# Kernel tuning notes

Measured on AMD Instinct MI355X. Metric: run time of the kernel, lower is better.

The kernel has to match this reference:

```python
import jax, jax.numpy as jnp
import numpy as np

N_HEAD = 16
RMS_EPS = 1.1920928955078125e-07  # torch F.rms_norm default eps = finfo(fp32).eps


def _rope_tables(seq_len, head_dim, dtype):
    steps = jnp.arange(seq_len, dtype=jnp.float32)
    rates = 10000.0 ** (-jnp.arange(0, head_dim, 2, dtype=jnp.float32) / head_dim)
    angles = jnp.outer(steps, rates)  # [S, D/2]
    return jnp.cos(angles).astype(dtype)[None, None], jnp.sin(angles).astype(dtype)[None, None]


def _apply_rotary(x, cos, sin):
    # interleaved RoPE: pairs (x[2i], x[2i+1]) rotated
    left = x[..., ::2]
    right = x[..., 1::2]
    lo = left * cos - right * sin
    ro = left * sin + right * cos
    return jnp.stack((lo, ro), axis=-1).reshape(x.shape)


def _rms_norm(x, eps=RMS_EPS):
    ms = jnp.mean(jnp.square(x), axis=-1, keepdims=True)
    return x * jax.lax.rsqrt(ms + eps)


def setup_inputs() -> dict:
    key = jax.random.key(0)
    k1, k2, k3 = jax.random.split(key, 3)
    B, S, E = 2, 2048, 2048
    x = jax.random.normal(k1, (B, S, E), dtype=jnp.float32)
    w_qkv = jax.random.normal(k2, (3 * E, E), dtype=jnp.float32) * (E ** -0.5)
    w_proj = jax.random.normal(k3, (E, E), dtype=jnp.float32) * (E ** -0.5)
    return {"x": x, "w_qkv": w_qkv, "w_proj": w_proj}


def reference(x, w_qkv, w_proj):
    B, S, E = x.shape
    H = N_HEAD
    D = E // H

    qkv = x @ w_qkv.T  # [B, S, 3E]
    q, k, v = jnp.split(qkv, 3, axis=-1)
    # [B, S, E] -> [B, H, S, D]
    q = q.reshape(B, S, H, D).transpose(0, 2, 1, 3)
    k = k.reshape(B, S, H, D).transpose(0, 2, 1, 3)
    v = v.reshape(B, S, H, D).transpose(0, 2, 1, 3)

    cos, sin = _rope_tables(S, D, x.dtype)  # [1,1,S,D/2]
    q = _apply_rotary(q, cos, sin)
    k = _apply_rotary(k, cos, sin)

    q = _rms_norm(q)
    k = _rms_norm(k)

    scale = 1.0 / jnp.sqrt(jnp.asarray(D, dtype=x.dtype))
    scores = jnp.einsum("bhqd,bhkd->bhqk", q, k) * scale  # [B,H,S,S]
    causal = jnp.tril(jnp.ones((S, S), dtype=bool))
    scores = jnp.where(causal[None, None], scores, jnp.asarray(-jnp.inf, dtype=scores.dtype))
    attn = jax.nn.softmax(scores, axis=-1)
    y = jnp.einsum("bhqk,bhkd->bhqd", attn, v)  # [B,H,S,D]
    y = y.transpose(0, 2, 1, 3).reshape(B, S, E)
    return y @ w_proj.T
```

## Files before the change

### kernel.cpp

```cpp
#include <hip/hip_runtime.h>

typedef unsigned short ushort_t;
using bf16x8 = __attribute__((ext_vector_type(8))) short;
using u16x8  = __attribute__((ext_vector_type(8))) unsigned short;
using f32x4  = __attribute__((ext_vector_type(4))) float;

#define DEV static __device__ __forceinline__

DEV unsigned short f2bf(float f) {
  union { float f; unsigned u; } a; a.f = f;
  unsigned r = a.u + 0x7fffu + ((a.u >> 16) & 1u);
  return (unsigned short)(r >> 16);
}
DEV float bf2f(unsigned short u) {
  union { unsigned u; float f; } a; a.u = ((unsigned)u) << 16;
  return a.f;
}
DEV void load_lds16(const void* g, void* l) {
  __builtin_amdgcn_global_load_lds(
      (const __attribute__((address_space(1))) void*)g,
      (__attribute__((address_space(3))) void*)l, 16, 0, 0);
}

__global__ __launch_bounds__(256) void cast_kernel(
    const float* __restrict__ src, ushort_t* __restrict__ dst, int n4) {
  int i = blockIdx.x * 256 + threadIdx.x;
  if (i >= n4) return;
  float4 f = ((const float4*)src)[i];
  ushort4 o;
  o.x = f2bf(f.x); o.y = f2bf(f.y); o.z = f2bf(f.z); o.w = f2bf(f.w);
  ((ushort4*)dst)[i] = o;
}

__global__ __launch_bounds__(256) void rope_tables_kernel(float* __restrict__ tab) {
  int idx = blockIdx.x * 256 + threadIdx.x;
  int s = idx >> 6, i = idx & 63;
  float rate = exp2f(-13.287712379549449f * ((float)(2 * i) * (1.0f / 128.0f)));
  float ang = (float)s * rate;
  tab[idx * 2]     = cosf(ang);
  tab[idx * 2 + 1] = sinf(ang);
}

template<int OUTF32>
__global__ __launch_bounds__(256) void gemm_bt(
    const ushort_t* __restrict__ A, const ushort_t* __restrict__ B,
    void* __restrict__ C, int M, int N, int K) {
  __shared__ __align__(16) ushort_t sA[128 * 32];
  __shared__ __align__(16) ushort_t sB[128 * 32];
  const int tid  = threadIdx.x;
  const int wave = tid >> 6;
  const int lane = tid & 63;
  const int lrow = lane & 15;
  const int lk   = lane >> 4;
  const int bm = blockIdx.y * 128;
  const int bn = blockIdx.x * 128;
  const int wrow = (wave >> 1) * 64;
  const int wcol = (wave & 1) * 64;

  f32x4 acc[4][4];
#pragma unroll
  for (int r = 0; r < 4; ++r)
#pragma unroll
    for (int c = 0; c < 4; ++c) acc[r][c] = (f32x4){0.f, 0.f, 0.f, 0.f};

  const int sRow0 = wave * 32 + (lane >> 2);
  const int sRow1 = sRow0 + 16;
  const int sSwz  = ((lane & 3) * 16) ^ ((sRow0 & 3) << 4);
  const char* aS0 = (const char*)A + (size_t)(bm + sRow0) * (size_t)(K * 2) + sSwz;
  const char* aS1 = (const char*)A + (size_t)(bm + sRow1) * (size_t)(K * 2) + sSwz;
  const char* bS0 = (const char*)B + (size_t)(bn + sRow0) * (size_t)(K * 2) + sSwz;
  const char* bS1 = (const char*)B + (size_t)(bn + sRow1) * (size_t)(K * 2) + sSwz;
  char* aD0 = (char*)sA + wave * 2048 + lane * 16;
  char* aD1 = aD0 + 1024;
  char* bD0 = (char*)sB + wave * 2048 + lane * 16;
  char* bD1 = bD0 + 1024;

  int offA[4], offB[4];
  const int fSwz = (lk * 16) ^ ((lrow & 3) << 4);
#pragma unroll
  for (int r = 0; r < 4; ++r) offA[r] = (wrow + r * 16 + lrow) * 64 + fSwz;
#pragma unroll
  for (int c = 0; c < 4; ++c) offB[c] = (wcol + c * 16 + lrow) * 64 + fSwz;

  const int nk = K >> 5;
  for (int ks = 0; ks < nk; ++ks) {
    const size_t koff = (size_t)ks * 64;
    load_lds16(aS0 + koff, aD0);
    load_lds16(aS1 + koff, aD1);
    load_lds16(bS0 + koff, bD0);
    load_lds16(bS1 + koff, bD1);
    __syncthreads();
    bf16x8 af[4], bv[4];
#pragma unroll
    for (int r = 0; r < 4; ++r) af[r] = *(const bf16x8*)((const char*)sA + offA[r]);
#pragma unroll
    for (int c = 0; c < 4; ++c) bv[c] = *(const bf16x8*)((const char*)sB + offB[c]);
#pragma unroll
    for (int r = 0; r < 4; ++r)
#pragma unroll
      for (int c = 0; c < 4; ++c)
        acc[r][c] = __builtin_amdgcn_mfma_f32_16x16x32_bf16(af[r], bv[c], acc[r][c], 0, 0, 0);
    __syncthreads();
  }

#pragma unroll
  for (int r = 0; r < 4; ++r)
#pragma unroll
    for (int i = 0; i < 4; ++i) {
      const size_t row = (size_t)(bm + wrow + r * 16 + lk * 4 + i);
#pragma unroll
      for (int c = 0; c < 4; ++c) {
        const size_t col = (size_t)(bn + wcol + c * 16 + lrow);
        float v = acc[r][c][i];
        if (OUTF32) ((float*)C)[row * (size_t)N + col] = v;
        else        ((ushort_t*)C)[row * (size_t)N + col] = f2bf(v);
      }
    }
}

__global__ __launch_bounds__(256) void rope_rms_kernel(
    const ushort_t* __restrict__ qkv, ushort_t* __restrict__ q,
    ushort_t* __restrict__ k, ushort_t* __restrict__ vt,
    const float* __restrict__ tab) {
  const int lane = threadIdx.x & 63;
  const int row  = blockIdx.x * 4 + (threadIdx.x >> 6);
  const int h = row & 15;
  int t = row >> 4;
  const int which = t % 3; t /= 3;
  const int s = t & 2047;
  const int b = t >> 11;
  const size_t src = ((size_t)(b * 2048 + s)) * 6144 + which * 2048 + h * 128 + lane * 2;
  ushort2 xv = *(const ushort2*)&qkv[src];
  if (which == 2) {
    size_t vbase = ((size_t)((b * 16 + h) * 128 + lane * 2)) * 2048 + s;
    vt[vbase]        = xv.x;
    vt[vbase + 2048] = xv.y;
    return;
  }
  float lo = bf2f(xv.x), ro = bf2f(xv.y);
  const float2 cs = *(const float2*)&tab[(s * 64 + lane) * 2];
  float l2 = lo * cs.x - ro * cs.y;
  float r2 = lo * cs.y + ro * cs.x;
  float ss = l2 * l2 + r2 * r2;
#pragma unroll
  for (int off = 1; off < 64; off <<= 1) ss += __shfl_xor(ss, off);
  float inv = rsqrtf(ss * (1.0f / 128.0f) + 1.1920928955078125e-07f);
  if (which == 0) inv *= 0.1275174398f;
  lo = l2 * inv; ro = r2 * inv;
  ushort_t* dst = (which == 0) ? q : k;
  ushort2 o; o.x = f2bf(lo); o.y = f2bf(ro);
  *(ushort2*)&dst[(((size_t)(b * 16 + h)) * 2048 + s) * 128 + lane * 2] = o;
}

__global__ __launch_bounds__(256) void attn_kernel(
    const ushort_t* __restrict__ Q, const ushort_t* __restrict__ K,
    const ushort_t* __restrict__ VT, ushort_t* __restrict__ Y) {
  __shared__ __align__(16) ushort_t sK[64 * 128];
  __shared__ __align__(16) ushort_t sV[128 * 64];
  const int bh = blockIdx.x;
  const int yp = blockIdx.y;
  const int wave = threadIdx.x >> 6, lane = threadIdx.x & 63;
  const int ql = lane & 15, lk = lane >> 4;
  const size_t hq = (size_t)bh * 2048 * 128;
  const int b = bh >> 4, h = bh & 15;

  const char* kB = (const char*)(K + hq);
  const char* vB = (const char*)(VT + hq);
  const char* kSrc[4]; char* kDst[4];
  const char* vSrc[4]; char* vDst[4];
#pragma unroll
  for (int t = 0; t < 4; ++t) {
    int r = wave * 16 + t * 4 + (lane >> 4);
    int kgr = r >> 4, lkr = (r >> 2) & 3, ir = r & 3;
    int rho = (kgr >> 1) * 32 + lkr * 8 + (kgr & 1) * 4 + ir;
    kSrc[t] = kB + rho * 256 + (((lane & 15) * 16) ^ ((r & 7) << 4));
    kDst[t] = (char*)sK + (wave * 256 + t * 64 + lane) * 16;
    int d = wave * 32 + t * 8 + (lane >> 3);
    vSrc[t] = vB + (size_t)d * 4096 + (((lane & 7) * 16) ^ ((d & 7) << 4));
    vDst[t] = (char*)sV + (wave * 256 + t * 64 + lane) * 16;
  }

  for (int pass = 0; pass < 2; ++pass) {
    const int qt = pass ? (31 - yp) : yp;
    const int q = qt * 64 + wave * 16 + ql;

    bf16x8 qf[4];
#pragma unroll
    for (int ks = 0; ks < 4; ++ks)
      qf[ks] = *(const bf16x8*)&Q[hq + (size_t)q * 128 + ks * 32 + lk * 8];

    f32x4 acc[8];
#pragma unroll
    for (int g = 0; g < 8; ++g) acc[g] = (f32x4){0.f, 0.f, 0.f, 0.f};
    float mrow = -3.0e38f, lsum = 0.f;

    for (int kt = 0; kt <= qt; ++kt) {
#pragma unroll
      for (int t = 0; t < 4; ++t) {
        load_lds16(kSrc[t] + (size_t)kt * 16384, kDst[t]);
        load_lds16(vSrc[t] + kt * 128, vDst[t]);
      }
      __syncthreads();

      f32x4 st[4];
#pragma unroll
      for (int kg = 0; kg < 4; ++kg) st[kg] = (f32x4){0.f, 0.f, 0.f, 0.f};
#pragma unroll
      for (int kg = 0; kg < 4; ++kg) {
        const int row = kg * 16 + ql;
        const int rswz = (row & 7) << 4;
#pragma unroll
        for (int ks = 0; ks < 4; ++ks) {
          bf16x8 kf = *(const bf16x8*)((const char*)sK + row * 256 + ((ks * 64 + lk * 16) ^ rswz));
          st[kg] = __builtin_amdgcn_mfma_f32_16x16x32_bf16(kf, qf[ks], st[kg], 0, 0, 0);
        }
      }
      float sv[4][4]; float mp = -3.0e38f;
#pragma unroll
      for (int kg = 0; kg < 4; ++kg) {
        const int kl = ((kg >> 1) << 5) + lk * 8 + ((kg & 1) << 2);
#pragma unroll
        for (int i = 0; i < 4; ++i) {
          const int key = kt * 64 + kl + i;
          float v = (key <= q) ? st[kg][i] : -3.0e38f;
          sv[kg][i] = v;
          mp = fmaxf(mp, v);
        }
      }
      mp = fmaxf(mp, __shfl_xor(mp, 16));
      mp = fmaxf(mp, __shfl_xor(mp, 32));
      const float mn = fmaxf(mrow, mp);
      const float corr = exp2f(mrow - mn);
      mrow = mn;
      float p[4][4]; float rs = 0.f;
#pragma unroll
      for (int kg = 0; kg < 4; ++kg)
#pragma unroll
        for (int i = 0; i < 4; ++i) {
          float e = exp2f(sv[kg][i] - mn);
          p[kg][i] = e; rs += e;
        }
      rs += __shfl_xor(rs, 16);
      rs += __shfl_xor(rs, 32);
      lsum = lsum * corr + rs;
#pragma unroll
      for (int g = 0; g < 8; ++g)
#pragma unroll
        for (int i = 0; i < 4; ++i) acc[g][i] *= corr;
      bf16x8 pb[2];
#pragma unroll
      for (int c = 0; c < 2; ++c) {
        union { bf16x8 v; ushort_t u[8]; } pk;
#pragma unroll
        for (int j = 0; j < 8; ++j) pk.u[j] = f2bf(p[2 * c + (j >> 2)][j & 3]);
        pb[c] = pk.v;
      }
#pragma unroll
      for (int dg = 0; dg < 8; ++dg) {
        const int d = dg * 16 + ql;
        const int dswz = (d & 7) << 4;
#pragma unroll
        for (int c = 0; c < 2; ++c) {
          bf16x8 vf = *(const bf16x8*)((const char*)sV + d * 128 + ((c * 64 + lk * 16) ^ dswz));
          acc[dg] = __builtin_amdgcn_mfma_f32_16x16x32_bf16(vf, pb[c], acc[dg], 0, 0, 0);
        }
      }
      __syncthreads();
    }

    const float inv = 1.0f / lsum;
    const size_t orow = ((size_t)(b * 2048 + q)) * 2048 + h * 128;
#pragma unroll
    for (int dg = 0; dg < 8; ++dg) {
      ushort4 o;
      o.x = f2bf(acc[dg][0] * inv);
      o.y = f2bf(acc[dg][1] * inv);
      o.z = f2bf(acc[dg][2] * inv);
      o.w = f2bf(acc[dg][3] * inv);
      *(ushort4*)&Y[orow + dg * 16 + lk * 4] = o;
    }
  }
}

extern "C" void kernel_launch(void* const* d_in, const int* in_sizes, int n_in,
                              void* d_out, int out_size, void* d_ws, size_t ws_size,
                              hipStream_t stream) {
  const float* x     = (const float*)d_in[0];
  const float* wqkv  = (const float*)d_in[1];
  const float* wproj = (const float*)d_in[2];
  float* out = (float*)d_out;
  char* ws = (char*)d_ws;

  ushort_t* x_bf     = (ushort_t*)(ws);
  ushort_t* wqkv_bf  = (ushort_t*)(ws + 16777216);
  ushort_t* wproj_bf = (ushort_t*)(ws + 41943040);
  ushort_t* qkv_bf   = (ushort_t*)(ws + 50331648);
  ushort_t* q_bf     = (ushort_t*)(ws + 100663296);
  ushort_t* k_bf     = (ushort_t*)(ws + 117440512);
  ushort_t* vt_bf    = (ushort_t*)(ws + 134217728);
  float*    tab      = (float*)(ws + 150994944);
  if (ws_size < 152043520u) return;

  cast_kernel<<<8192, 256, 0, stream>>>(x, x_bf, 2097152);
  cast_kernel<<<12288, 256, 0, stream>>>(wqkv, wqkv_bf, 3145728);
  cast_kernel<<<4096, 256, 0, stream>>>(wproj, wproj_bf, 1048576);
  rope_tables_kernel<<<512, 256, 0, stream>>>(tab);

  gemm_bt<0><<<dim3(48, 32), 256, 0, stream>>>(x_bf, wqkv_bf, qkv_bf, 4096, 6144, 2048);

  rope_rms_kernel<<<49152, 256, 0, stream>>>(qkv_bf, q_bf, k_bf, vt_bf, tab);

  attn_kernel<<<dim3(32, 16), 256, 0, stream>>>(q_bf, k_bf, vt_bf, qkv_bf );

  gemm_bt<1><<<dim3(16, 32), 256, 0, stream>>>(qkv_bf, wproj_bf, out, 4096, 2048, 2048);
}
```

Baseline: 344.7 us.

## Double-buffer GEMM and attention loads, enlarge tiles, remap GEMM workgroups

Replaces the GEMM with a templated kernel that double-buffers LDS tiles, so the next K-slice is fetched while MFMAs run. It uses a 256x128 tile for the QKV projection, remaps workgroup IDs for cache locality, and raises wave priority around the MFMA block. The attention kernel also double-buffers K/V tiles and has each wave process two 16-query groups (128 queries per block), reusing each K/V fragment across both. This cuts LDS traffic and sync stalls per FLOP, at the cost of more registers and LDS and lower occupancy.

```diff
diff --git a/kernel.cpp b/kernel.cpp
--- a/kernel.cpp
+++ b/kernel.cpp
@@ -2,7 +2,6 @@
 
 typedef unsigned short ushort_t;
 using bf16x8 = __attribute__((ext_vector_type(8))) short;
-using u16x8  = __attribute__((ext_vector_type(8))) unsigned short;
 using f32x4  = __attribute__((ext_vector_type(4))) float;
 
 #define DEV static __device__ __forceinline__
@@ -41,77 +40,106 @@
   tab[idx * 2 + 1] = sinf(ang);
 }
 
-template<int OUTF32>
-__global__ __launch_bounds__(256) void gemm_bt(
-    const ushort_t* __restrict__ A, const ushort_t* __restrict__ B,
+template<int BM, int BN, int OUTF32>
+__global__ __launch_bounds__(256, 2) void gemm_bal(
+    const ushort_t* __restrict__ A, const ushort_t* __restrict__ Bm,
     void* __restrict__ C, int M, int N, int K) {
-  __shared__ __align__(16) ushort_t sA[128 * 32];
-  __shared__ __align__(16) ushort_t sB[128 * 32];
-  const int tid  = threadIdx.x;
+  constexpr int MF   = BM / 32;
+  constexpr int NF   = BN / 32;
+  constexpr int NCA  = BM / 64;
+  constexpr int NCB  = BN / 64;
+  constexpr int NC   = NCA + NCB;
+  constexpr int ABY  = BM * 64;
+  constexpr int BUFB = (BM + BN) * 64;
+  __shared__ __align__(16) char lds[2 * BUFB];
+
+  const int nby = M / BM;
+  const int nwg = nby * (N / BN);
+  const int orig = blockIdx.x;
+  const int wgid = (orig & 7) * (nwg >> 3) + (orig >> 3);
+  const int bm = (wgid % nby) * BM;
+  const int bn = (wgid / nby) * BN;
+
+  const int tid = threadIdx.x;
+  const int lane = tid & 63;
   const int wave = tid >> 6;
-  const int lane = tid & 63;
-  const int lrow = lane & 15;
-  const int lk   = lane >> 4;
-  const int bm = blockIdx.y * 128;
-  const int bn = blockIdx.x * 128;
-  const int wrow = (wave >> 1) * 64;
-  const int wcol = (wave & 1) * 64;
-
-  f32x4 acc[4][4];
-#pragma unroll
-  for (int r = 0; r < 4; ++r)
-#pragma unroll
-    for (int c = 0; c < 4; ++c) acc[r][c] = (f32x4){0.f, 0.f, 0.f, 0.f};
-
-  const int sRow0 = wave * 32 + (lane >> 2);
-  const int sRow1 = sRow0 + 16;
-  const int sSwz  = ((lane & 3) * 16) ^ ((sRow0 & 3) << 4);
-  const char* aS0 = (const char*)A + (size_t)(bm + sRow0) * (size_t)(K * 2) + sSwz;
-  const char* aS1 = (const char*)A + (size_t)(bm + sRow1) * (size_t)(K * 2) + sSwz;
-  const char* bS0 = (const char*)B + (size_t)(bn + sRow0) * (size_t)(K * 2) + sSwz;
-  const char* bS1 = (const char*)B + (size_t)(bn + sRow1) * (size_t)(K * 2) + sSwz;
-  char* aD0 = (char*)sA + wave * 2048 + lane * 16;
-  char* aD1 = aD0 + 1024;
-  char* bD0 = (char*)sB + wave * 2048 + lane * 16;
-  char* bD1 = bD0 + 1024;
-
-  int offA[4], offB[4];
-  const int fSwz = (lk * 16) ^ ((lrow & 3) << 4);
-#pragma unroll
-  for (int r = 0; r < 4; ++r) offA[r] = (wrow + r * 16 + lrow) * 64 + fSwz;
-#pragma unroll
-  for (int c = 0; c < 4; ++c) offB[c] = (wcol + c * 16 + lrow) * 64 + fSwz;
-
-  const int nk = K >> 5;
-  for (int ks = 0; ks < nk; ++ks) {
-    const size_t koff = (size_t)ks * 64;
-    load_lds16(aS0 + koff, aD0);
-    load_lds16(aS1 + koff, aD1);
-    load_lds16(bS0 + koff, bD0);
-    load_lds16(bS1 + koff, bD1);
+  const int ql = lane & 15, lk = lane >> 4;
+  const int wm = wave >> 1, wn = wave & 1;
+
+  f32x4 acc[MF][NF];
+#pragma unroll
+  for (int m = 0; m < MF; ++m)
+#pragma unroll
+    for (int n = 0; n < NF; ++n) acc[m][n] = (f32x4){0.f, 0.f, 0.f, 0.f};
+
+  const int rin  = tid >> 2;
+  const int sswz = ((tid & 3) ^ ((rin >> 1) & 3)) * 16;
+  const size_t rb = (size_t)K * 2;
+  const char* src[NC];
+#pragma unroll
+  for (int c = 0; c < NCA; ++c)
+    src[c] = (const char*)A + (size_t)(bm + c * 64 + rin) * rb + sswz;
+#pragma unroll
+  for (int c = 0; c < NCB; ++c)
+    src[NCA + c] = (const char*)Bm + (size_t)(bn + c * 64 + rin) * rb + sswz;
+  char* const ldsc = (char*)lds;
+  const int dT = tid * 16;
+
+  int aOff[MF], bOff[NF];
+#pragma unroll
+  for (int m = 0; m < MF; ++m) {
+    const int r = wm * (BM / 2) + m * 16 + ql;
+    aOff[m] = r * 64 + ((lk ^ ((r >> 1) & 3)) * 16);
+  }
+#pragma unroll
+  for (int n = 0; n < NF; ++n) {
+    const int r = wn * (BN / 2) + n * 16 + ql;
+    bOff[n] = ABY + r * 64 + ((lk ^ ((r >> 1) & 3)) * 16);
+  }
+
+#define STAGE(BB, KT) do {                                   \
+    char* d_ = ldsc + (BB) * BUFB + dT;                      \
+    const size_t ko_ = (size_t)(KT) * 64;                    \
+    _Pragma("unroll")                                        \
+    for (int c = 0; c < NC; ++c)                             \
+      load_lds16(src[c] + ko_, d_ + c * 4096);               \
+  } while (0)
+#define MFMA(a, b, c) __builtin_amdgcn_mfma_f32_16x16x32_bf16(a, b, c, 0, 0, 0)
+
+  const int ns = K >> 5;
+  STAGE(0, 0);
+  __syncthreads();
+
+  for (int t = 0; t < ns; ++t) {
+    const int nk = (t + 1 < ns) ? t + 1 : t;
+    STAGE((t + 1) & 1, nk);
+    const char* sb = ldsc + (t & 1) * BUFB;
+    bf16x8 bF[NF], aF[MF];
+#pragma unroll
+    for (int n = 0; n < NF; ++n) bF[n] = *(const bf16x8*)(sb + bOff[n]);
+#pragma unroll
+    for (int m = 0; m < MF; ++m) aF[m] = *(const bf16x8*)(sb + aOff[m]);
+    __builtin_amdgcn_s_setprio(1);
+#pragma unroll
+    for (int m = 0; m < MF; ++m)
+#pragma unroll
+      for (int n = 0; n < NF; ++n)
+        acc[m][n] = MFMA(aF[m], bF[n], acc[m][n]);
+    __builtin_amdgcn_s_setprio(0);
     __syncthreads();
-    bf16x8 af[4], bv[4];
-#pragma unroll
-    for (int r = 0; r < 4; ++r) af[r] = *(const bf16x8*)((const char*)sA + offA[r]);
-#pragma unroll
-    for (int c = 0; c < 4; ++c) bv[c] = *(const bf16x8*)((const char*)sB + offB[c]);
-#pragma unroll
-    for (int r = 0; r < 4; ++r)
-#pragma unroll
-      for (int c = 0; c < 4; ++c)
-        acc[r][c] = __builtin_amdgcn_mfma_f32_16x16x32_bf16(af[r], bv[c], acc[r][c], 0, 0, 0);
-    __syncthreads();
-  }
-
-#pragma unroll
-  for (int r = 0; r < 4; ++r)
+  }
+#undef STAGE
+#undef MFMA
+
+#pragma unroll
+  for (int m = 0; m < MF; ++m)
 #pragma unroll
     for (int i = 0; i < 4; ++i) {
-      const size_t row = (size_t)(bm + wrow + r * 16 + lk * 4 + i);
-#pragma unroll
-      for (int c = 0; c < 4; ++c) {
-        const size_t col = (size_t)(bn + wcol + c * 16 + lrow);
-        float v = acc[r][c][i];
+      const size_t row = (size_t)(bm + wm * (BM / 2) + m * 16 + lk * 4 + i);
+#pragma unroll
+      for (int n = 0; n < NF; ++n) {
+        const size_t col = (size_t)(bn + wn * (BN / 2) + n * 16 + ql);
+        float v = acc[m][n][i];
         if (OUTF32) ((float*)C)[row * (size_t)N + col] = v;
         else        ((ushort_t*)C)[row * (size_t)N + col] = f2bf(v);
       }
@@ -152,11 +180,11 @@
   *(ushort2*)&dst[(((size_t)(b * 16 + h)) * 2048 + s) * 128 + lane * 2] = o;
 }
 
-__global__ __launch_bounds__(256) void attn_kernel(
+__global__ __launch_bounds__(256, 1) void attn_kernel(
     const ushort_t* __restrict__ Q, const ushort_t* __restrict__ K,
     const ushort_t* __restrict__ VT, ushort_t* __restrict__ Y) {
-  __shared__ __align__(16) ushort_t sK[64 * 128];
-  __shared__ __align__(16) ushort_t sV[128 * 64];
+  __shared__ __align__(16) ushort_t sK[2][64 * 128];
+  __shared__ __align__(16) ushort_t sV[2][128 * 64];
   const int bh = blockIdx.x;
   const int yp = blockIdx.y;
   const int wave = threadIdx.x >> 6, lane = threadIdx.x & 63;
@@ -180,80 +208,102 @@
     vDst[t] = (char*)sV + (wave * 256 + t * 64 + lane) * 16;
   }
 
+#define STAGEKV(KT, BB) do {                                         \
+    _Pragma("unroll")                                                \
+    for (int t_ = 0; t_ < 4; ++t_) {                                 \
+      load_lds16(kSrc[t_] + (size_t)(KT) * 16384, kDst[t_] + (BB) * 16384); \
+      load_lds16(vSrc[t_] + (KT) * 128, vDst[t_] + (BB) * 16384);    \
+    }                                                                \
+  } while (0)
+
+  int buf = 0;
+  STAGEKV(0, 0);
+  __syncthreads();
+
   for (int pass = 0; pass < 2; ++pass) {
-    const int qt = pass ? (31 - yp) : yp;
-    const int q = qt * 64 + wave * 16 + ql;
-
-    bf16x8 qf[4];
-#pragma unroll
-    for (int ks = 0; ks < 4; ++ks)
-      qf[ks] = *(const bf16x8*)&Q[hq + (size_t)q * 128 + ks * 32 + lk * 8];
-
-    f32x4 acc[8];
-#pragma unroll
-    for (int g = 0; g < 8; ++g) acc[g] = (f32x4){0.f, 0.f, 0.f, 0.f};
-    float mrow = -3.0e38f, lsum = 0.f;
-
-    for (int kt = 0; kt <= qt; ++kt) {
-#pragma unroll
-      for (int t = 0; t < 4; ++t) {
-        load_lds16(kSrc[t] + (size_t)kt * 16384, kDst[t]);
-        load_lds16(vSrc[t] + kt * 128, vDst[t]);
-      }
-      __syncthreads();
-
-      f32x4 st[4];
-#pragma unroll
-      for (int kg = 0; kg < 4; ++kg) st[kg] = (f32x4){0.f, 0.f, 0.f, 0.f};
+    const int qt = pass ? (15 - yp) : yp;
+    const int ktmax = 2 * qt + 1;
+    const int q0 = qt * 128 + wave * 32 + ql;
+
+    bf16x8 qf[2][4];
+#pragma unroll
+    for (int g = 0; g < 2; ++g)
+#pragma unroll
+      for (int ks = 0; ks < 4; ++ks)
+        qf[g][ks] = *(const bf16x8*)&Q[hq + (size_t)(q0 + g * 16) * 128 + ks * 32 + lk * 8];
+
+    f32x4 acc[2][8];
+#pragma unroll
+    for (int g = 0; g < 2; ++g)
+#pragma unroll
+      for (int dg = 0; dg < 8; ++dg) acc[g][dg] = (f32x4){0.f, 0.f, 0.f, 0.f};
+    float mrow[2] = {-3.0e38f, -3.0e38f}, lsum[2] = {0.f, 0.f};
+
+    for (int kt = 0; kt <= ktmax; ++kt) {
+      const int nk = (kt < ktmax) ? kt + 1 : (pass == 0 ? 0 : ktmax);
+      STAGEKV(nk, buf ^ 1);
+      const char* sKb = (const char*)sK + buf * 16384;
+      const char* sVb = (const char*)sV + buf * 16384;
+
+      f32x4 st[2][4];
+#pragma unroll
+      for (int g = 0; g < 2; ++g)
+#pragma unroll
+        for (int kg = 0; kg < 4; ++kg) st[g][kg] = (f32x4){0.f, 0.f, 0.f, 0.f};
 #pragma unroll
       for (int kg = 0; kg < 4; ++kg) {
         const int row = kg * 16 + ql;
         const int rswz = (row & 7) << 4;
 #pragma unroll
         for (int ks = 0; ks < 4; ++ks) {
-          bf16x8 kf = *(const bf16x8*)((const char*)sK + row * 256 + ((ks * 64 + lk * 16) ^ rswz));
-          st[kg] = __builtin_amdgcn_mfma_f32_16x16x32_bf16(kf, qf[ks], st[kg], 0, 0, 0);
+          bf16x8 kf = *(const bf16x8*)(sKb + row * 256 + ((ks * 64 + lk * 16) ^ rswz));
+          st[0][kg] = __builtin_amdgcn_mfma_f32_16x16x32_bf16(kf, qf[0][ks], st[0][kg], 0, 0, 0);
+          st[1][kg] = __builtin_amdgcn_mfma_f32_16x16x32_bf16(kf, qf[1][ks], st[1][kg], 0, 0, 0);
         }
       }
-      float sv[4][4]; float mp = -3.0e38f;
-#pragma unroll
-      for (int kg = 0; kg < 4; ++kg) {
-        const int kl = ((kg >> 1) << 5) + lk * 8 + ((kg & 1) << 2);
-#pragma unroll
-        for (int i = 0; i < 4; ++i) {
-          const int key = kt * 64 + kl + i;
-          float v = (key <= q) ? st[kg][i] : -3.0e38f;
-          sv[kg][i] = v;
-          mp = fmaxf(mp, v);
+      bf16x8 pb[2][2];
+#pragma unroll
+      for (int g = 0; g < 2; ++g) {
+        const int q = q0 + g * 16;
+        float sv[4][4]; float mp = -3.0e38f;
+#pragma unroll
+        for (int kg = 0; kg < 4; ++kg) {
+          const int kl = ((kg >> 1) << 5) + lk * 8 + ((kg & 1) << 2);
+#pragma unroll
+          for (int i = 0; i < 4; ++i) {
+            const int key = kt * 64 + kl + i;
+            float v = (key <= q) ? st[g][kg][i] : -3.0e38f;
+            sv[kg][i] = v;
+            mp = fmaxf(mp, v);
+          }
         }
-      }
-      mp = fmaxf(mp, __shfl_xor(mp, 16));
-      mp = fmaxf(mp, __shfl_xor(mp, 32));
-      const float mn = fmaxf(mrow, mp);
-      const float corr = exp2f(mrow - mn);
-      mrow = mn;
-      float p[4][4]; float rs = 0.f;
-#pragma unroll
-      for (int kg = 0; kg < 4; ++kg)
-#pragma unroll
-        for (int i = 0; i < 4; ++i) {
-          float e = exp2f(sv[kg][i] - mn);
-          p[kg][i] = e; rs += e;
+        mp = fmaxf(mp, __shfl_xor(mp, 16));
+        mp = fmaxf(mp, __shfl_xor(mp, 32));
+        const float mn = fmaxf(mrow[g], mp);
+        const float corr = exp2f(mrow[g] - mn);
+        mrow[g] = mn;
+        float p[4][4]; float rs = 0.f;
+#pragma unroll
+        for (int kg = 0; kg < 4; ++kg)
+#pragma unroll
+          for (int i = 0; i < 4; ++i) {
+            float e = exp2f(sv[kg][i] - mn);
+            p[kg][i] = e; rs += e;
+          }
+        rs += __shfl_xor(rs, 16);
+        rs += __shfl_xor(rs, 32);
+        lsum[g] = lsum[g] * corr + rs;
+#pragma unroll
+        for (int dg = 0; dg < 8; ++dg)
+#pragma unroll
+          for (int i = 0; i < 4; ++i) acc[g][dg][i] *= corr;
+#pragma unroll
+        for (int c = 0; c < 2; ++c) {
+          union { bf16x8 v; ushort_t u[8]; } pk;
+#pragma unroll
+          for (int j = 0; j < 8; ++j) pk.u[j] = f2bf(p[2 * c + (j >> 2)][j & 3]);
+          pb[g][c] = pk.v;
         }
-      rs += __shfl_xor(rs, 16);
-      rs += __shfl_xor(rs, 32);
-      lsum = lsum * corr + rs;
-#pragma unroll
-      for (int g = 0; g < 8; ++g)
-#pragma unroll
-        for (int i = 0; i < 4; ++i) acc[g][i] *= corr;
-      bf16x8 pb[2];
-#pragma unroll
-      for (int c = 0; c < 2; ++c) {
-        union { bf16x8 v; ushort_t u[8]; } pk;
-#pragma unroll
-        for (int j = 0; j < 8; ++j) pk.u[j] = f2bf(p[2 * c + (j >> 2)][j & 3]);
-        pb[c] = pk.v;
       }
 #pragma unroll
       for (int dg = 0; dg < 8; ++dg) {
@@ -261,25 +311,31 @@
         const int dswz = (d & 7) << 4;
 #pragma unroll
         for (int c = 0; c < 2; ++c) {
-          bf16x8 vf = *(const bf16x8*)((const char*)sV + d * 128 + ((c * 64 + lk * 16) ^ dswz));
-          acc[dg] = __builtin_amdgcn_mfma_f32_16x16x32_bf16(vf, pb[c], acc[dg], 0, 0, 0);
+          bf16x8 vf = *(const bf16x8*)(sVb + d * 128 + ((c * 64 + lk * 16) ^ dswz));
+          acc[0][dg] = __builtin_amdgcn_mfma_f32_16x16x32_bf16(vf, pb[0][c], acc[0][dg], 0, 0, 0);
+          acc[1][dg] = __builtin_amdgcn_mfma_f32_16x16x32_bf16(vf, pb[1][c], acc[1][dg], 0, 0, 0);
         }
       }
       __syncthreads();
+      buf ^= 1;
     }
 
-    const float inv = 1.0f / lsum;
-    const size_t orow = ((size_t)(b * 2048 + q)) * 2048 + h * 128;
-#pragma unroll
-    for (int dg = 0; dg < 8; ++dg) {
-      ushort4 o;
-      o.x = f2bf(acc[dg][0] * inv);
-      o.y = f2bf(acc[dg][1] * inv);
-      o.z = f2bf(acc[dg][2] * inv);
-      o.w = f2bf(acc[dg][3] * inv);
-      *(ushort4*)&Y[orow + dg * 16 + lk * 4] = o;
+#pragma unroll
+    for (int g = 0; g < 2; ++g) {
+      const float inv = 1.0f / lsum[g];
+      const size_t orow = ((size_t)(b * 2048 + q0 + g * 16)) * 2048 + h * 128;
+#pragma unroll
+      for (int dg = 0; dg < 8; ++dg) {
+        ushort4 o;
+        o.x = f2bf(acc[g][dg][0] * inv);
+        o.y = f2bf(acc[g][dg][1] * inv);
+        o.z = f2bf(acc[g][dg][2] * inv);
+        o.w = f2bf(acc[g][dg][3] * inv);
+        *(ushort4*)&Y[orow + dg * 16 + lk * 4] = o;
+      }
     }
   }
+#undef STAGEKV
 }
 
 extern "C" void kernel_launch(void* const* d_in, const int* in_sizes, int n_in,
@@ -306,11 +362,11 @@
   cast_kernel<<<4096, 256, 0, stream>>>(wproj, wproj_bf, 1048576);
   rope_tables_kernel<<<512, 256, 0, stream>>>(tab);
 
-  gemm_bt<0><<<dim3(48, 32), 256, 0, stream>>>(x_bf, wqkv_bf, qkv_bf, 4096, 6144, 2048);
+  gemm_bal<256, 128, 0><<<768, 256, 0, stream>>>(x_bf, wqkv_bf, qkv_bf, 4096, 6144, 2048);
 
   rope_rms_kernel<<<49152, 256, 0, stream>>>(qkv_bf, q_bf, k_bf, vt_bf, tab);
 
-  attn_kernel<<<dim3(32, 16), 256, 0, stream>>>(q_bf, k_bf, vt_bf, qkv_bf );
-
-  gemm_bt<1><<<dim3(16, 32), 256, 0, stream>>>(qkv_bf, wproj_bf, out, 4096, 2048, 2048);
-}
+  attn_kernel<<<dim3(32, 8), 256, 0, stream>>>(q_bf, k_bf, vt_bf, qkv_bf );
+
+  gemm_bal<128, 128, 1><<<512, 256, 0, stream>>>(qkv_bf, wproj_bf, out, 4096, 2048, 2048);
+}
```

After: 339.8 us. About the same (-1.4%).
